# Kernel tuning notes

Measured on AMD Instinct MI355X. Metric: run time of the kernel, lower is better.

Reference implementation:

```python
import jax, jax.numpy as jnp
import numpy as np

B, S, D = 1024, 48, 256   # graphs, nodes-per-graph, embedding dim (= input_dim)
GDIM = 512                # graph_dim
N = B * S                 # total nodes
E = 4 * N                 # directed edges (avg degree ~4, molecular graphs)
W_SCALE = 0.05


def setup_inputs() -> dict:
    key = jax.random.key(0)
    ks = jax.random.split(key, 8)
    return {
        "sub2gene_out": jax.random.normal(ks[0], (B, S, D), jnp.float32),
        "edge_index": jax.random.randint(ks[1], (2, E), 0, N, dtype=jnp.int64),
        # conv1: in_channels = 2*D (concat of x and laplacian-smoothed x)
        "W_l1": jax.random.normal(ks[2], (GDIM, 2 * D), jnp.float32) * W_SCALE,
        "W_r1": jax.random.normal(ks[3], (GDIM, 2 * D), jnp.float32) * W_SCALE,
        "b1": jnp.zeros((GDIM,), jnp.float32),
        # conv2: graph_dim -> graph_dim
        "W_l2": jax.random.normal(ks[4], (GDIM, GDIM), jnp.float32) * W_SCALE,
        "W_r2": jax.random.normal(ks[5], (GDIM, GDIM), jnp.float32) * W_SCALE,
        "b2": jnp.zeros((GDIM,), jnp.float32),
    }


def sage_conv(x, src, dst, W_l, W_r, b, n):
    """PyG SAGEConv (mean aggregation, root_weight=True):
    out_i = W_l @ mean_{j in N(i)} x_j + W_r @ x_i + b, messages flow src->dst."""
    msg = x[src]                                            # [E, F] gather
    agg = jax.ops.segment_sum(msg, dst, num_segments=n)     # [N, F]
    cnt = jax.ops.segment_sum(jnp.ones((src.shape[0],), x.dtype), dst, num_segments=n)
    mean = agg / jnp.maximum(cnt, 1.0)[:, None]
    return mean @ W_l.T + x @ W_r.T + b


def reference(sub2gene_out, edge_index, W_l1, W_r1, b1, W_l2, W_r2, b2):
    b_, s_, d_ = sub2gene_out.shape
    n = b_ * s_
    x = sub2gene_out.reshape(n, d_)                         # cat of per-graph node features
    row, col = edge_index[0], edge_index[1]

    # sym-normalized Laplacian L = I - D^{-1/2} A D^{-1/2}; lap_x = L @ x
    ones_e = jnp.ones((row.shape[0],), x.dtype)
    deg = jax.ops.segment_sum(ones_e, row, num_segments=n)
    dinv = jnp.where(deg > 0, 1.0, 0.0) / jnp.sqrt(jnp.maximum(deg, 1.0))
    w = -(dinv[row] * dinv[col])                            # off-diagonal -A_norm
    lap_x = x + jax.ops.segment_sum(w[:, None] * x[col], row, num_segments=n)

    x_comb = jnp.concatenate([x, lap_x], axis=-1)           # [N, 2D]
    h = jax.nn.gelu(sage_conv(x_comb, row, col, W_l1, W_r1, b1, n), approximate=False)
    h = sage_conv(h, row, col, W_l2, W_r2, b2, n)           # [N, GDIM]

    # global_mean_pool: every graph has exactly s_ nodes
    batch = jnp.repeat(jnp.arange(b_), s_)
    pooled = jax.ops.segment_sum(h, batch, num_segments=b_) / jnp.asarray(s_, h.dtype)
    return pooled                                           # [B, GDIM]
```

## Files before the change

### kernel.cpp

```cpp
#include <hip/hip_runtime.h>
#include <math.h>

typedef unsigned short u16;
typedef __attribute__((ext_vector_type(8))) short bf16x8;
typedef __attribute__((ext_vector_type(4))) float f32x4;

#define NB 1024
#define NS 48
#define ND 256
#define NN (NB*NS)
#define NE (4*NN)
#define GD 512
#define KK 1024

__device__ __forceinline__ void gld16(const void* g, void* l) {
  __builtin_amdgcn_global_load_lds(
      (const __attribute__((address_space(1))) void*)(void*)g,
      (__attribute__((address_space(3))) void*)l, 16, 0, 0);
}

__device__ __forceinline__ float bf2f(u16 h) {
  unsigned u = ((unsigned)h) << 16; float f; __builtin_memcpy(&f, &u, 4); return f;
}
__device__ __forceinline__ u16 f2bf(float f) {
  unsigned u; __builtin_memcpy(&u, &f, 4);
  u += 0x7fffu + ((u >> 16) & 1u);
  return (u16)(u >> 16);
}
__device__ __forceinline__ void unpack8(uint4 v, float* f) {
  f[0]=bf2f((u16)(v.x & 0xffff)); f[1]=bf2f((u16)(v.x >> 16));
  f[2]=bf2f((u16)(v.y & 0xffff)); f[3]=bf2f((u16)(v.y >> 16));
  f[4]=bf2f((u16)(v.z & 0xffff)); f[5]=bf2f((u16)(v.z >> 16));
  f[6]=bf2f((u16)(v.w & 0xffff)); f[7]=bf2f((u16)(v.w >> 16));
}
__device__ __forceinline__ uint4 pack8(const float* f) {
  uint4 v;
  v.x = (unsigned)f2bf(f[0]) | ((unsigned)f2bf(f[1]) << 16);
  v.y = (unsigned)f2bf(f[2]) | ((unsigned)f2bf(f[3]) << 16);
  v.z = (unsigned)f2bf(f[4]) | ((unsigned)f2bf(f[5]) << 16);
  v.w = (unsigned)f2bf(f[6]) | ((unsigned)f2bf(f[7]) << 16);
  return v;
}


__global__ void k_hist(const int* __restrict__ ei, int* __restrict__ deg, int* __restrict__ cnt) {
  int e = blockIdx.x * 256 + threadIdx.x;
  if (e < NE) {
    atomicAdd(&deg[ei[e]], 1);
    atomicAdd(&cnt[ei[NE + e]], 1);
  }
}

__global__ void k_exscan2(const int* __restrict__ deg, const int* __restrict__ cnt,
                          int* __restrict__ rowOff, int* __restrict__ colOff,
                          float* __restrict__ dinv) {
  const int t = threadIdx.x;
  const int base = t * 48;
  if (blockIdx.x == 2) {
    for (int i = 0; i < 48; ++i) {
      int d = deg[base + i];
      dinv[base + i] = (d > 0) ? rsqrtf((float)d) : 0.0f;
    }
    return;
  }
  __shared__ int sums[1024];
  const int* in = blockIdx.x ? cnt : deg;
  int* out = blockIdx.x ? colOff : rowOff;
  int s = 0;
  for (int i = 0; i < 48; ++i) s += in[base + i];
  sums[t] = s;
  __syncthreads();
  for (int off = 1; off < 1024; off <<= 1) {
    int v = (t >= off) ? sums[t - off] : 0;
    __syncthreads();
    sums[t] += v;
    __syncthreads();
  }
  int run = (t == 0) ? 0 : sums[t - 1];
  for (int i = 0; i < 48; ++i) { int v = in[base + i]; out[base + i] = run; run += v; }
  if (t == 1023) out[NN] = run;
}

__global__ void k_fill(const int* __restrict__ ei,
                       const int* __restrict__ rowOff, const int* __restrict__ colOff,
                       int* __restrict__ rowFill, int* __restrict__ colFill,
                       int* __restrict__ rowCol, int* __restrict__ colSrc) {
  int e = blockIdx.x * 256 + threadIdx.x;
  if (e < NE) {
    int r = ei[e], c = ei[NE + e];
    int pr = atomicAdd(&rowFill[r], 1);
    rowCol[rowOff[r] + pr] = c;
    int pc = atomicAdd(&colFill[c], 1);
    colSrc[colOff[c] + pc] = r;
  }
}

__global__ void k_wx(const float* __restrict__ Wr1, const float* __restrict__ Wl1,
                     const float* __restrict__ Wr2, const float* __restrict__ Wl2,
                     u16* __restrict__ W1c, u16* __restrict__ W2c,
                     const float* __restrict__ x, u16* __restrict__ xcomb) {
  const int b = blockIdx.x;
  if (b < 1024) {
    const float* Wr = (b < 512) ? Wr1 : Wr2;
    const float* Wl = (b < 512) ? Wl1 : Wl2;
    u16* Wc = (b < 512) ? W1c : W2c;
    int i = ((b & 511) * 256 + threadIdx.x) * 4;
    int n = i >> 10, k = i & 1023;
    const float* src = (k < 512) ? (Wr + n * 512 + k) : (Wl + n * 512 + (k - 512));
    float4 v = *(const float4*)src;
    ushort4 h; h.x = f2bf(v.x); h.y = f2bf(v.y); h.z = f2bf(v.z); h.w = f2bf(v.w);
    *(ushort4*)(Wc + i) = h;
  } else {
    int i = ((b - 1024) * 256 + threadIdx.x) * 8;
    int node = i >> 8, col = i & 255;
    float4 v0 = *(const float4*)(x + i);
    float4 v1 = *(const float4*)(x + i + 4);
    float f[8] = {v0.x, v0.y, v0.z, v0.w, v1.x, v1.y, v1.z, v1.w};
    *(uint4*)(xcomb + (size_t)node * KK + col) = pack8(f);
  }
}

__global__ void k_lap(u16* __restrict__ xcomb, const int* __restrict__ rowOff,
                      const int* __restrict__ rowCol, const float* __restrict__ dinv) {
  const int gid = blockIdx.x * 256 + threadIdx.x;
  const int wid = gid >> 6, lane = gid & 63;
  const int node = wid * 2 + (lane >> 5);
  const int f0 = (lane & 31) * 8;
  float xi[8]; unpack8(*(const uint4*)(xcomb + (size_t)node * KK + f0), xi);
  float a[8] = {};
  const int s0 = rowOff[node], s1 = rowOff[node + 1];
  for (int p = s0; p < s1; p += 4) {
    const int q1 = (p + 1 < s1) ? p + 1 : s1 - 1;
    const int q2 = (p + 2 < s1) ? p + 2 : s1 - 1;
    const int q3 = (p + 3 < s1) ? p + 3 : s1 - 1;
    const int c0 = rowCol[p], c1 = rowCol[q1], c2 = rowCol[q2], c3 = rowCol[q3];
    const float w0 = dinv[c0];
    const float w1 = (p + 1 < s1) ? dinv[c1] : 0.f;
    const float w2 = (p + 2 < s1) ? dinv[c2] : 0.f;
    const float w3 = (p + 3 < s1) ? dinv[c3] : 0.f;
    float g0[8], g1[8], g2[8], g3[8];
    unpack8(*(const uint4*)(xcomb + (size_t)c0 * KK + f0), g0);
    unpack8(*(const uint4*)(xcomb + (size_t)c1 * KK + f0), g1);
    unpack8(*(const uint4*)(xcomb + (size_t)c2 * KK + f0), g2);
    unpack8(*(const uint4*)(xcomb + (size_t)c3 * KK + f0), g3);
    #pragma unroll
    for (int j = 0; j < 8; ++j) a[j] += w0 * g0[j] + w1 * g1[j] + w2 * g2[j] + w3 * g3[j];
  }
  const float di = dinv[node];
  float l[8];
  #pragma unroll
  for (int j = 0; j < 8; ++j) l[j] = xi[j] - di * a[j];
  *(uint4*)(xcomb + (size_t)node * KK + ND + f0) = pack8(l);
}

__global__ void k_aggx(u16* __restrict__ xcomb, const int* __restrict__ colOff,
                       const int* __restrict__ colSrc) {
  const int gid = blockIdx.x * 256 + threadIdx.x;
  const int wid = gid >> 6, lane = gid & 63;
  const int n0 = wid * 2, n1 = n0 + 1;
  const int f0 = lane * 8;
  const int sA = colOff[n0], sB = colOff[n0 + 1], eB = colOff[n1 + 1];
  const int dA = sB - sA, dB = eB - sB;
  float accA[8] = {}, accB[8] = {};
  const int T = (dA > dB) ? dA : dB;
  for (int t = 0; t < T; t += 4) {
    int cA[4], cB[4];
    float wA[4], wB[4];
    #pragma unroll
    for (int i = 0; i < 4; ++i) {
      const int o = t + i;
      int vA = colSrc[sA + ((o < dA) ? o : 0)];
      cA[i] = (o < dA) ? vA : 0;  wA[i] = (o < dA) ? 1.f : 0.f;
      int vB = colSrc[sB + ((o < dB) ? o : 0)];
      cB[i] = (o < dB) ? vB : 0;  wB[i] = (o < dB) ? 1.f : 0.f;
    }
    uint4 gA[4], gB[4];
    #pragma unroll
    for (int i = 0; i < 4; ++i) {
      gA[i] = *(const uint4*)(xcomb + (size_t)cA[i] * KK + f0);
      gB[i] = *(const uint4*)(xcomb + (size_t)cB[i] * KK + f0);
    }
    #pragma unroll
    for (int i = 0; i < 4; ++i) {
      float tmp[8];
      unpack8(gA[i], tmp);
      #pragma unroll
      for (int j = 0; j < 8; ++j) accA[j] += wA[i] * tmp[j];
      unpack8(gB[i], tmp);
      #pragma unroll
      for (int j = 0; j < 8; ++j) accB[j] += wB[i] * tmp[j];
    }
  }
  const float invA = (dA > 0) ? 1.0f / (float)dA : 1.0f;
  const float invB = (dB > 0) ? 1.0f / (float)dB : 1.0f;
  float rA[8], rB[8];
  #pragma unroll
  for (int j = 0; j < 8; ++j) { rA[j] = accA[j] * invA; rB[j] = accB[j] * invB; }
  *(uint4*)(xcomb + (size_t)n0 * KK + 512 + f0) = pack8(rA);
  *(uint4*)(xcomb + (size_t)n1 * KK + 512 + f0) = pack8(rB);
}

template <int MODE>
__global__ __launch_bounds__(256, 4) void k_gemm(const u16* __restrict__ A,
                                                 const u16* __restrict__ Bw,
                                                 const float* __restrict__ bias,
                                                 void* __restrict__ OutP) {
  __shared__ u16 As[128 * 64];
  __shared__ u16 Bs[128 * 64];
  const int tid = threadIdx.x;
  const int w = tid >> 6, lane = tid & 63;
  const int wr = w >> 1, wc = w & 1;

  const int cpx = gridDim.x >> 3;
  const int o = blockIdx.x;
  const int swz = (o & 7) * cpx + (o >> 3);
  const int bx = swz >> 2;
  const int by = swz & 3;

  const int lrow = lane >> 3;
  const int lcol = ((lane & 7) ^ lrow) * 8;
  const u16* Ag = A  + (size_t)(bx * 128 + w * 32 + lrow) * KK + lcol;
  const u16* Bg = Bw + (size_t)(by * 128 + w * 32 + lrow) * KK + lcol;
  u16* Asl = As + w * 32 * 64;
  u16* Bsl = Bs + w * 32 * 64;

  const int kg = lane >> 4;
  const int aoff = (wr * 64 + (lane & 15)) * 64 + ((kg ^ (lane & 7)) * 8);
  const int boff = (wc * 64 + (lane & 15)) * 64 + ((kg ^ (lane & 7)) * 8);

  f32x4 acc[4][4] = {};

  for (int kt = 0; kt < KK; kt += 64) {
    #pragma unroll
    for (int c = 0; c < 4; ++c) {
      gld16(Ag + kt + c * 8 * KK, Asl + c * 8 * 64);
      gld16(Bg + kt + c * 8 * KK, Bsl + c * 8 * 64);
    }
    __syncthreads();
    #pragma unroll
    for (int s2 = 0; s2 < 2; ++s2) {
      const int flip = s2 * 32;
      bf16x8 aF[4], bF[4];
      #pragma unroll
      for (int i = 0; i < 4; ++i) aF[i] = *(const bf16x8*)(As + ((aoff + i * 1024) ^ flip));
      #pragma unroll
      for (int i = 0; i < 4; ++i) bF[i] = *(const bf16x8*)(Bs + ((boff + i * 1024) ^ flip));
      #pragma unroll
      for (int mi = 0; mi < 4; ++mi)
        #pragma unroll
        for (int ni = 0; ni < 4; ++ni)
          acc[mi][ni] = __builtin_amdgcn_mfma_f32_16x16x32_bf16(aF[mi], bF[ni], acc[mi][ni], 0, 0, 0);
    }
    __syncthreads();
  }

  const int lc = lane & 15, lr = (lane >> 4) * 4;
  const size_t r0 = (size_t)bx * 128 + wr * 64;
  const int cb = by * 128 + wc * 64;
  float bv[4];
  #pragma unroll
  for (int ni = 0; ni < 4; ++ni) bv[ni] = bias[cb + ni * 16 + lc];
  #pragma unroll
  for (int mi = 0; mi < 4; ++mi)
    #pragma unroll
    for (int ni = 0; ni < 4; ++ni)
      #pragma unroll
      for (int r = 0; r < 4; ++r) {
        float v = acc[mi][ni][r] + bv[ni];
        const size_t idx = (r0 + mi * 16 + lr + r) * GD + (cb + ni * 16 + lc);
        if (MODE == 0) {
          v = 0.5f * v * (1.0f + erff(v * 0.70710678118654752f));
          ((u16*)OutP)[idx] = f2bf(v);
        } else {
          ((float*)OutP)[idx] = v;
        }
      }
}

__global__ __launch_bounds__(512) void k_aggh(const u16* __restrict__ h, const int* __restrict__ colOff,
                                              const int* __restrict__ colSrc,
                                              u16* __restrict__ h2cat) {
  __shared__ float red[2][8][GD];
  const int g = blockIdx.x;
  const int t = threadIdx.x, w = t >> 6, lane = t & 63;
  const int f0 = lane * 8;
  float pr[8] = {}, pa[8] = {};
  for (int n = w; n < NS; n += 16) {
    const int node0 = g * NS + n, node1 = node0 + 8;
    float tmp[8];
    unpack8(*(const uint4*)(h + (size_t)node0 * GD + f0), tmp);
    #pragma unroll
    for (int j = 0; j < 8; ++j) pr[j] += tmp[j];
    unpack8(*(const uint4*)(h + (size_t)node1 * GD + f0), tmp);
    #pragma unroll
    for (int j = 0; j < 8; ++j) pr[j] += tmp[j];
    const int sA = colOff[node0], eA = colOff[node0 + 1];
    const int sB = colOff[node1], eB = colOff[node1 + 1];
    const int dA = eA - sA, dB = eB - sB;
    float accA[8] = {}, accB[8] = {};
    const int T = (dA > dB) ? dA : dB;
    for (int p = 0; p < T; p += 4) {
      int cA[4], cB[4];
      float wA[4], wB[4];
      #pragma unroll
      for (int i = 0; i < 4; ++i) {
        const int oo = p + i;
        int vA = colSrc[sA + ((oo < dA) ? oo : 0)];
        cA[i] = (oo < dA) ? vA : 0;  wA[i] = (oo < dA) ? 1.f : 0.f;
        int vB = colSrc[sB + ((oo < dB) ? oo : 0)];
        cB[i] = (oo < dB) ? vB : 0;  wB[i] = (oo < dB) ? 1.f : 0.f;
      }
      uint4 gA[4], gB[4];
      #pragma unroll
      for (int i = 0; i < 4; ++i) {
        gA[i] = *(const uint4*)(h + (size_t)cA[i] * GD + f0);
        gB[i] = *(const uint4*)(h + (size_t)cB[i] * GD + f0);
      }
      #pragma unroll
      for (int i = 0; i < 4; ++i) {
        unpack8(gA[i], tmp);
        #pragma unroll
        for (int j = 0; j < 8; ++j) accA[j] += wA[i] * tmp[j];
        unpack8(gB[i], tmp);
        #pragma unroll
        for (int j = 0; j < 8; ++j) accB[j] += wB[i] * tmp[j];
      }
    }
    const float invA = (dA > 0) ? 1.0f / (float)dA : 1.0f;
    const float invB = (dB > 0) ? 1.0f / (float)dB : 1.0f;
    #pragma unroll
    for (int j = 0; j < 8; ++j) pa[j] += accA[j] * invA;
    #pragma unroll
    for (int j = 0; j < 8; ++j) pa[j] += accB[j] * invB;
  }
  #pragma unroll
  for (int j = 0; j < 8; ++j) { red[0][w][f0 + j] = pr[j]; red[1][w][f0 + j] = pa[j]; }
  __syncthreads();
  if (t < 256) {
    const int f = t * 2;
    const float invS = 1.0f / (float)NS;
    float r0 = 0.f, r1 = 0.f, a0 = 0.f, a1 = 0.f;
    #pragma unroll
    for (int ww = 0; ww < 8; ++ww) {
      r0 += red[0][ww][f]; r1 += red[0][ww][f + 1];
      a0 += red[1][ww][f]; a1 += red[1][ww][f + 1];
    }
    r0 *= invS; r1 *= invS; a0 *= invS; a1 *= invS;
    *(unsigned*)(h2cat + (size_t)g * KK + f)       = (unsigned)f2bf(r0) | ((unsigned)f2bf(r1) << 16);
    *(unsigned*)(h2cat + (size_t)g * KK + 512 + f) = (unsigned)f2bf(a0) | ((unsigned)f2bf(a1) << 16);
  }
}

extern "C" void kernel_launch(void* const* d_in, const int* in_sizes, int n_in,
                              void* d_out, int out_size, void* d_ws, size_t ws_size,
                              hipStream_t stream) {
  const float* x   = (const float*)d_in[0];
  const int*   ei  = (const int*)d_in[1];
  const float* Wl1 = (const float*)d_in[2];
  const float* Wr1 = (const float*)d_in[3];
  const float* b1  = (const float*)d_in[4];
  const float* Wl2 = (const float*)d_in[5];
  const float* Wr2 = (const float*)d_in[6];
  const float* b2  = (const float*)d_in[7];
  float* out = (float*)d_out;
  (void)in_sizes; (void)n_in; (void)out_size; (void)ws_size;

  int* deg     = (int*)d_ws;
  int* cnt     = deg + NN;
  int* rowFill = cnt + NN;
  int* colFill = rowFill + NN;
  int* rowOff  = colFill + NN;
  int* colOff  = rowOff + NN + 64;
  float* dinv  = (float*)(colOff + NN + 64);
  int* rowCol  = (int*)(dinv + NN);
  int* colSrc  = rowCol + NE;
  u16* W1c     = (u16*)(colSrc + NE);
  u16* W2c     = W1c + 512 * KK;
  u16* h2cat   = W2c + 512 * KK;
  u16* xcomb   = h2cat + (size_t)NB * KK;
  u16* h       = xcomb + (size_t)NN * KK;

  hipMemsetAsync(deg, 0, sizeof(int) * 4 * NN, stream);

  k_hist<<<NE / 256, 256, 0, stream>>>(ei, deg, cnt);
  k_exscan2<<<3, 1024, 0, stream>>>(deg, cnt, rowOff, colOff, dinv);
  k_fill<<<NE / 256, 256, 0, stream>>>(ei, rowOff, colOff, rowFill, colFill, rowCol, colSrc);
  k_wx<<<1024 + (NN * ND) / (256 * 8), 256, 0, stream>>>(Wr1, Wl1, Wr2, Wl2, W1c, W2c, x, xcomb);
  k_lap<<<(NN * 32) / 256, 256, 0, stream>>>(xcomb, rowOff, rowCol, dinv);
  k_aggx<<<(NN * 32) / 256, 256, 0, stream>>>(xcomb, colOff, colSrc);

  k_gemm<0><<<(NN / 128) * 4, 256, 0, stream>>>(xcomb, W1c, b1, (void*)h);

  k_aggh<<<NB, 512, 0, stream>>>(h, colOff, colSrc, h2cat);

  k_gemm<1><<<(NB / 128) * 4, 256, 0, stream>>>(h2cat, W2c, b2, (void*)out);
}
```

Baseline: 251.1 us.

## Fuse histogram with conversion, split-K the second GEMM, widen first GEMM blocks

Merges the edge-degree histogram kernel into the weight/feature bf16 conversion kernel, which removes one launch. The first GEMM moves to 512-thread blocks with 8 waves, each computing a 64x32 sub-tile, to raise the number of waves per block. The second GEMM, which had only 32 blocks, is split along K into 8 slices across 256 blocks that accumulate into a pre-zeroed output with float atomics. This adds an output memset and atomic traffic, and makes the fp32 summation order nondeterministic.

```diff
diff --git a/kernel.cpp b/kernel.cpp
--- a/kernel.cpp
+++ b/kernel.cpp
@@ -42,12 +42,34 @@
   return v;
 }
 
-
-__global__ void k_hist(const int* __restrict__ ei, int* __restrict__ deg, int* __restrict__ cnt) {
-  int e = blockIdx.x * 256 + threadIdx.x;
-  if (e < NE) {
+__global__ void k_wxh(const int* __restrict__ ei, int* __restrict__ deg, int* __restrict__ cnt,
+                      const float* __restrict__ Wr1, const float* __restrict__ Wl1,
+                      const float* __restrict__ Wr2, const float* __restrict__ Wl2,
+                      u16* __restrict__ W1c, u16* __restrict__ W2c,
+                      const float* __restrict__ x, u16* __restrict__ xcomb) {
+  const int b = blockIdx.x;
+  if (b < 768) {
+    int e = b * 256 + threadIdx.x;
     atomicAdd(&deg[ei[e]], 1);
     atomicAdd(&cnt[ei[NE + e]], 1);
+  } else if (b < 1792) {
+    const int b2 = b - 768;
+    const float* Wr = (b2 < 512) ? Wr1 : Wr2;
+    const float* Wl = (b2 < 512) ? Wl1 : Wl2;
+    u16* Wc = (b2 < 512) ? W1c : W2c;
+    int i = ((b2 & 511) * 256 + threadIdx.x) * 4;
+    int n = i >> 10, k = i & 1023;
+    const float* src = (k < 512) ? (Wr + n * 512 + k) : (Wl + n * 512 + (k - 512));
+    float4 v = *(const float4*)src;
+    ushort4 h; h.x = f2bf(v.x); h.y = f2bf(v.y); h.z = f2bf(v.z); h.w = f2bf(v.w);
+    *(ushort4*)(Wc + i) = h;
+  } else {
+    int i = ((b - 1792) * 256 + threadIdx.x) * 8;
+    int node = i >> 8, col = i & 255;
+    float4 v0 = *(const float4*)(x + i);
+    float4 v1 = *(const float4*)(x + i + 4);
+    float f[8] = {v0.x, v0.y, v0.z, v0.w, v1.x, v1.y, v1.z, v1.w};
+    *(uint4*)(xcomb + (size_t)node * KK + col) = pack8(f);
   }
 }
 
@@ -92,31 +114,6 @@
     rowCol[rowOff[r] + pr] = c;
     int pc = atomicAdd(&colFill[c], 1);
     colSrc[colOff[c] + pc] = r;
-  }
-}
-
-__global__ void k_wx(const float* __restrict__ Wr1, const float* __restrict__ Wl1,
-                     const float* __restrict__ Wr2, const float* __restrict__ Wl2,
-                     u16* __restrict__ W1c, u16* __restrict__ W2c,
-                     const float* __restrict__ x, u16* __restrict__ xcomb) {
-  const int b = blockIdx.x;
-  if (b < 1024) {
-    const float* Wr = (b < 512) ? Wr1 : Wr2;
-    const float* Wl = (b < 512) ? Wl1 : Wl2;
-    u16* Wc = (b < 512) ? W1c : W2c;
-    int i = ((b & 511) * 256 + threadIdx.x) * 4;
-    int n = i >> 10, k = i & 1023;
-    const float* src = (k < 512) ? (Wr + n * 512 + k) : (Wl + n * 512 + (k - 512));
-    float4 v = *(const float4*)src;
-    ushort4 h; h.x = f2bf(v.x); h.y = f2bf(v.y); h.z = f2bf(v.z); h.w = f2bf(v.w);
-    *(ushort4*)(Wc + i) = h;
-  } else {
-    int i = ((b - 1024) * 256 + threadIdx.x) * 8;
-    int node = i >> 8, col = i & 255;
-    float4 v0 = *(const float4*)(x + i);
-    float4 v1 = *(const float4*)(x + i + 4);
-    float f[8] = {v0.x, v0.y, v0.z, v0.w, v1.x, v1.y, v1.z, v1.w};
-    *(uint4*)(xcomb + (size_t)node * KK + col) = pack8(f);
   }
 }
 
@@ -200,27 +197,95 @@
   *(uint4*)(xcomb + (size_t)n1 * KK + 512 + f0) = pack8(rB);
 }
 
-template <int MODE>
-__global__ __launch_bounds__(256, 4) void k_gemm(const u16* __restrict__ A,
-                                                 const u16* __restrict__ Bw,
-                                                 const float* __restrict__ bias,
-                                                 void* __restrict__ OutP) {
+__global__ __launch_bounds__(512, 4) void k_gemm1(const u16* __restrict__ A,
+                                                  const u16* __restrict__ Bw,
+                                                  const float* __restrict__ bias,
+                                                  u16* __restrict__ Out) {
+  __shared__ u16 As[128 * 64];
+  __shared__ u16 Bs[128 * 64];
+  const int tid = threadIdx.x;
+  const int w = tid >> 6, lane = tid & 63;
+  const int wr = w >> 2, wc = w & 3;
+
+  const int cpx = gridDim.x >> 3;
+  const int o = blockIdx.x;
+  const int swz = (o & 7) * cpx + (o >> 3);
+  const int bx = swz >> 2;
+  const int by = swz & 3;
+
+  const int lrow = lane >> 3;
+  const int lcol = ((lane & 7) ^ lrow) * 8;
+  const u16* Ag = A  + (size_t)(bx * 128 + w * 16 + lrow) * KK + lcol;
+  const u16* Bg = Bw + (size_t)(by * 128 + w * 16 + lrow) * KK + lcol;
+  u16* Asl = As + w * 16 * 64;
+  u16* Bsl = Bs + w * 16 * 64;
+
+  const int kg = lane >> 4;
+  const int aoff = (wr * 64 + (lane & 15)) * 64 + ((kg ^ (lane & 7)) * 8);
+  const int boff = (wc * 32 + (lane & 15)) * 64 + ((kg ^ (lane & 7)) * 8);
+
+  f32x4 acc[4][2] = {};
+
+  for (int kt = 0; kt < KK; kt += 64) {
+    gld16(Ag + kt, Asl);
+    gld16(Ag + kt + 8 * KK, Asl + 8 * 64);
+    gld16(Bg + kt, Bsl);
+    gld16(Bg + kt + 8 * KK, Bsl + 8 * 64);
+    __syncthreads();
+    #pragma unroll
+    for (int s2 = 0; s2 < 2; ++s2) {
+      const int flip = s2 * 32;
+      bf16x8 aF[4], bF[2];
+      #pragma unroll
+      for (int i = 0; i < 4; ++i) aF[i] = *(const bf16x8*)(As + ((aoff + i * 1024) ^ flip));
+      #pragma unroll
+      for (int i = 0; i < 2; ++i) bF[i] = *(const bf16x8*)(Bs + ((boff + i * 1024) ^ flip));
+      #pragma unroll
+      for (int mi = 0; mi < 4; ++mi)
+        #pragma unroll
+        for (int ni = 0; ni < 2; ++ni)
+          acc[mi][ni] = __builtin_amdgcn_mfma_f32_16x16x32_bf16(aF[mi], bF[ni], acc[mi][ni], 0, 0, 0);
+    }
+    __syncthreads();
+  }
+
+  const int lc = lane & 15, lr = (lane >> 4) * 4;
+  const size_t r0 = (size_t)bx * 128 + wr * 64;
+  const int cb = by * 128 + wc * 32;
+  float bv[2];
+  #pragma unroll
+  for (int ni = 0; ni < 2; ++ni) bv[ni] = bias[cb + ni * 16 + lc];
+  #pragma unroll
+  for (int mi = 0; mi < 4; ++mi)
+    #pragma unroll
+    for (int ni = 0; ni < 2; ++ni)
+      #pragma unroll
+      for (int r = 0; r < 4; ++r) {
+        float v = acc[mi][ni][r] + bv[ni];
+        v = 0.5f * v * (1.0f + erff(v * 0.70710678118654752f));
+        Out[(r0 + mi * 16 + lr + r) * GD + (cb + ni * 16 + lc)] = f2bf(v);
+      }
+}
+
+__global__ __launch_bounds__(256, 4) void k_gemm2(const u16* __restrict__ A,
+                                                  const u16* __restrict__ Bw,
+                                                  const float* __restrict__ bias,
+                                                  float* __restrict__ Out) {
   __shared__ u16 As[128 * 64];
   __shared__ u16 Bs[128 * 64];
   const int tid = threadIdx.x;
   const int w = tid >> 6, lane = tid & 63;
   const int wr = w >> 1, wc = w & 1;
-
-  const int cpx = gridDim.x >> 3;
-  const int o = blockIdx.x;
-  const int swz = (o & 7) * cpx + (o >> 3);
-  const int bx = swz >> 2;
-  const int by = swz & 3;
+  const int bid = blockIdx.x;
+  const int ks = bid >> 5;
+  const int rr = bid & 31;
+  const int bx = rr >> 2;
+  const int by = rr & 3;
 
   const int lrow = lane >> 3;
   const int lcol = ((lane & 7) ^ lrow) * 8;
-  const u16* Ag = A  + (size_t)(bx * 128 + w * 32 + lrow) * KK + lcol;
-  const u16* Bg = Bw + (size_t)(by * 128 + w * 32 + lrow) * KK + lcol;
+  const u16* Ag = A  + (size_t)(bx * 128 + w * 32 + lrow) * KK + lcol + ks * 128;
+  const u16* Bg = Bw + (size_t)(by * 128 + w * 32 + lrow) * KK + lcol + ks * 128;
   u16* Asl = As + w * 32 * 64;
   u16* Bsl = Bs + w * 32 * 64;
 
@@ -230,7 +295,8 @@
 
   f32x4 acc[4][4] = {};
 
-  for (int kt = 0; kt < KK; kt += 64) {
+  #pragma unroll
+  for (int kt = 0; kt < 128; kt += 64) {
     #pragma unroll
     for (int c = 0; c < 4; ++c) {
       gld16(Ag + kt + c * 8 * KK, Asl + c * 8 * 64);
@@ -259,22 +325,15 @@
   const int cb = by * 128 + wc * 64;
   float bv[4];
   #pragma unroll
-  for (int ni = 0; ni < 4; ++ni) bv[ni] = bias[cb + ni * 16 + lc];
+  for (int ni = 0; ni < 4; ++ni) bv[ni] = (ks == 0) ? bias[cb + ni * 16 + lc] : 0.0f;
   #pragma unroll
   for (int mi = 0; mi < 4; ++mi)
     #pragma unroll
     for (int ni = 0; ni < 4; ++ni)
       #pragma unroll
-      for (int r = 0; r < 4; ++r) {
-        float v = acc[mi][ni][r] + bv[ni];
-        const size_t idx = (r0 + mi * 16 + lr + r) * GD + (cb + ni * 16 + lc);
-        if (MODE == 0) {
-          v = 0.5f * v * (1.0f + erff(v * 0.70710678118654752f));
-          ((u16*)OutP)[idx] = f2bf(v);
-        } else {
-          ((float*)OutP)[idx] = v;
-        }
-      }
+      for (int r = 0; r < 4; ++r)
+        atomicAdd(&Out[(r0 + mi * 16 + lr + r) * GD + (cb + ni * 16 + lc)],
+                  acc[mi][ni][r] + bv[ni]);
 }
 
 __global__ __launch_bounds__(512) void k_aggh(const u16* __restrict__ h, const int* __restrict__ colOff,
@@ -381,17 +440,17 @@
   u16* h       = xcomb + (size_t)NN * KK;
 
   hipMemsetAsync(deg, 0, sizeof(int) * 4 * NN, stream);
-
-  k_hist<<<NE / 256, 256, 0, stream>>>(ei, deg, cnt);
+  hipMemsetAsync(out, 0, (size_t)NB * GD * sizeof(float), stream);
+
+  k_wxh<<<7936, 256, 0, stream>>>(ei, deg, cnt, Wr1, Wl1, Wr2, Wl2, W1c, W2c, x, xcomb);
   k_exscan2<<<3, 1024, 0, stream>>>(deg, cnt, rowOff, colOff, dinv);
   k_fill<<<NE / 256, 256, 0, stream>>>(ei, rowOff, colOff, rowFill, colFill, rowCol, colSrc);
-  k_wx<<<1024 + (NN * ND) / (256 * 8), 256, 0, stream>>>(Wr1, Wl1, Wr2, Wl2, W1c, W2c, x, xcomb);
   k_lap<<<(NN * 32) / 256, 256, 0, stream>>>(xcomb, rowOff, rowCol, dinv);
   k_aggx<<<(NN * 32) / 256, 256, 0, stream>>>(xcomb, colOff, colSrc);
 
-  k_gemm<0><<<(NN / 128) * 4, 256, 0, stream>>>(xcomb, W1c, b1, (void*)h);
+  k_gemm1<<<(NN / 128) * 4, 512, 0, stream>>>(xcomb, W1c, b1, h);
 
   k_aggh<<<NB, 512, 0, stream>>>(h, colOff, colSrc, h2cat);
 
-  k_gemm<1><<<(NB / 128) * 4, 256, 0, stream>>>(h2cat, W2c, b2, (void*)out);
-}
+  k_gemm2<<<256, 256, 0, stream>>>(h2cat, W2c, b2, out);
+}
```

New measurement: 246.6 us. About the same (-1.8%).
